# Optimization experiments

Measured on AMD Instinct MI355X. Metric: run time of the kernel, lower is better.

The kernel has to match this reference:

```python
import jax, jax.numpy as jnp
import numpy as np

H, D = 16, 64  # num_attention_heads, attention_head_size
BASE = 10000.0

def _rope(q, k, seq_len):
    # RotaryPositionalEmbedding: inv_freq over arange(0, D, 2); emb = cat(freqs, freqs)
    inv_freq = 1.0 / (BASE ** (jnp.arange(0, D, 2, dtype=jnp.float32) / D))  # [D/2]=32
    pos = jnp.arange(seq_len, dtype=jnp.float32)
    freqs = jnp.outer(pos, inv_freq)            # [S, 32]; equals cos_emb[..., :d]
    cos, sin = jnp.cos(freqs), jnp.sin(freqs)   # [S, 32]
    d = D // 2                                   # 32: only first half of head dim rotated
    half = d // 2                                # 16: internal rotate-half within rot part
    def rot(x):  # x: [B, H, S, D]
        xr, xp = x[..., :d], x[..., d:]
        swapped = jnp.concatenate([xr[..., half:], xr[..., :half]], axis=-1)
        xr2 = xr * cos - swapped * sin
        return jnp.concatenate([xr2, xp], axis=-1)
    return rot(q), rot(k)

def setup_inputs() -> dict:
    key = jax.random.key(0)
    ks = jax.random.split(key, 9)
    B, S, E = 2, 2048, 1024
    std = 0.02  # initializer_range
    inp = {"hidden_states": jax.random.normal(ks[0], (B, S, E), jnp.float32)}
    for i, n in enumerate(["q", "k", "v", "d"]):
        inp[f"W{n}"] = jax.random.normal(ks[1 + 2 * i], (E, E), jnp.float32) * std
        inp[f"b{n}"] = jnp.zeros((E,), jnp.float32)
    return inp

def reference(hidden_states, Wq, bq, Wk, bk, Wv, bv, Wd, bd):
    B, S, E = hidden_states.shape
    def heads(x):  # [B,S,E] -> [B,H,S,D]
        return x.reshape(B, S, H, D).transpose(0, 2, 1, 3)
    q = heads(hidden_states @ Wq + bq)
    k = heads(hidden_states @ Wk + bk)
    v = heads(hidden_states @ Wv + bv)
    q, k = _rope(q, k, S)
    scores = jnp.einsum("bhqd,bhkd->bhqk", q, k) / jnp.sqrt(jnp.float32(D))
    causal = jnp.tril(jnp.ones((S, S), dtype=bool))
    scores = jnp.where(causal, scores, -jnp.inf)
    probs = jax.nn.softmax(scores, axis=-1)
    ctx = jnp.einsum("bhqk,bhkd->bhqd", probs, v)
    ctx = ctx.transpose(0, 2, 1, 3).reshape(B, S, E)
    return ctx @ Wd + bd
```

## Files before the change

### kernel.cpp

```cpp
#include <hip/hip_runtime.h>
#include <stdint.h>

typedef __bf16 bf8 __attribute__((ext_vector_type(8)));
typedef float f4 __attribute__((ext_vector_type(4)));
typedef float f16v __attribute__((ext_vector_type(16)));
typedef unsigned short us8 __attribute__((ext_vector_type(8)));
typedef unsigned short us4 __attribute__((ext_vector_type(4)));

#define MFMA16(a, b, c) __builtin_amdgcn_mfma_f32_16x16x32_bf16(a, b, c, 0, 0, 0)
#define MFMA32(a, b, c) __builtin_amdgcn_mfma_f32_32x32x16_bf16(a, b, c, 0, 0, 0)

__device__ __forceinline__ unsigned short f2b(float f) {
  union { float f; unsigned u; } x; x.f = f;
  unsigned u = x.u;
  u += 0x7fffu + ((u >> 16) & 1u);
  return (unsigned short)(u >> 16);
}

__device__ __forceinline__ unsigned pk2(float a, float b) {
  union { float f; unsigned u; } ua, ub; ua.f = a; ub.f = b;
  return __builtin_amdgcn_perm(ub.u + 0x8000u, ua.u + 0x8000u, 0x07060302u);
}

__device__ __forceinline__ void gload16(const void* g, void* l) {
  __builtin_amdgcn_global_load_lds(
      (const __attribute__((address_space(1))) void*)g,
      (__attribute__((address_space(3))) void*)l, 16, 0, 0);
}

__global__ __launch_bounds__(256) void prep_kernel(
    const float* __restrict__ W0, const float* __restrict__ W1,
    const float* __restrict__ W2, const float* __restrict__ W3,
    unsigned short* __restrict__ T0, unsigned short* __restrict__ T1,
    unsigned short* __restrict__ T2, unsigned short* __restrict__ T3,
    const float* __restrict__ hid, unsigned short* __restrict__ hb) {
  if (blockIdx.z == 4) {
    int bi = blockIdx.x + 32 * blockIdx.y;
#pragma unroll
    for (int k = 0; k < 4; ++k) {
      int i = bi * 1024 + k * 256 + threadIdx.x;
      float4 v = ((const float4*)hid)[i];
      us4 r = { f2b(v.x), f2b(v.y), f2b(v.z), f2b(v.w) };
      *(us4*)(hb + (size_t)i * 4) = r;
    }
    return;
  }
  const float* W; unsigned short* Wt;
  if (blockIdx.z == 0)      { W = W0; Wt = T0; }
  else if (blockIdx.z == 1) { W = W1; Wt = T1; }
  else if (blockIdx.z == 2) { W = W2; Wt = T2; }
  else                      { W = W3; Wt = T3; }
  __shared__ float tile[32][33];
  int tx = threadIdx.x & 31, ty = threadIdx.x >> 5;
  int kb = blockIdx.x * 32, nb = blockIdx.y * 32;
#pragma unroll
  for (int j = 0; j < 32; j += 8)
    tile[ty + j][tx] = W[(size_t)(kb + ty + j) * 1024 + nb + tx];
  __syncthreads();
#pragma unroll
  for (int j = 0; j < 32; j += 8)
    Wt[(size_t)(nb + ty + j) * 1024 + kb + tx] = f2b(tile[tx][ty + j]);
}

__global__ __launch_bounds__(256) void gemm_qkv_kernel(
    const unsigned short* __restrict__ X,
    const unsigned short* __restrict__ Wqt, const unsigned short* __restrict__ Wkt,
    const unsigned short* __restrict__ Wvt,
    const float* __restrict__ bq, const float* __restrict__ bk,
    const float* __restrict__ bv,
    unsigned short* __restrict__ Qo, unsigned short* __restrict__ Ko,
    unsigned short* __restrict__ Vo) {
  const unsigned short* Wt; const float* bias; unsigned short* out;
  if (blockIdx.z == 0)      { Wt = Wqt; bias = bq; out = Qo; }
  else if (blockIdx.z == 1) { Wt = Wkt; bias = bk; out = Ko; }
  else                      { Wt = Wvt; bias = bv; out = Vo; }

  __shared__ unsigned short As[128 * 32];
  __shared__ unsigned short Bs[128 * 32];
  const int t = threadIdx.x;
  const int wave = t >> 6, lane = t & 63, quad = lane >> 4, l16 = lane & 15;
  const int wm = (wave >> 1) * 64, wn = (wave & 1) * 64;
  const int m0 = blockIdx.y * 128, n0 = blockIdx.x * 128;

  f4 acc[4][4];
#pragma unroll
  for (int mi = 0; mi < 4; ++mi)
#pragma unroll
    for (int ni = 0; ni < 4; ++ni) acc[mi][ni] = (f4)0.0f;

  for (int k0 = 0; k0 < 1024; k0 += 32) {
    __syncthreads();
#pragma unroll
    for (int it = 0; it < 2; ++it) {
      int chunk = it * 256 + wave * 64 + lane;
      int row = chunk >> 2, c = chunk & 3;
      gload16(&X[(size_t)(m0 + row) * 1024 + k0 + c * 8],
              &As[(size_t)(it * 256 + wave * 64) * 8]);
      gload16(&Wt[(size_t)(n0 + row) * 1024 + k0 + c * 8],
              &Bs[(size_t)(it * 256 + wave * 64) * 8]);
    }
    __syncthreads();
    bf8 a[4], b[4];
#pragma unroll
    for (int mi = 0; mi < 4; ++mi)
      a[mi] = *(const bf8*)&As[(wm + mi * 16 + l16) * 32 + quad * 8];
#pragma unroll
    for (int ni = 0; ni < 4; ++ni)
      b[ni] = *(const bf8*)&Bs[(wn + ni * 16 + l16) * 32 + quad * 8];
#pragma unroll
    for (int mi = 0; mi < 4; ++mi)
#pragma unroll
      for (int ni = 0; ni < 4; ++ni)
        acc[mi][ni] = MFMA16(a[mi], b[ni], acc[mi][ni]);
  }

  float biasv[4];
#pragma unroll
  for (int ni = 0; ni < 4; ++ni) biasv[ni] = bias[n0 + wn + ni * 16 + l16];

  if (blockIdx.z < 2) {
    const float kr = 13.287712379549449f / 32.0f;
    const float f0 = exp2f(-(float)l16 * kr);
    const float f1 = exp2f(-(float)(l16 + 16) * kr);
    const float qs = (blockIdx.z == 0) ? 0.18033688011112042f : 1.0f;
#pragma unroll
    for (int mi = 0; mi < 4; ++mi) {
#pragma unroll
      for (int r = 0; r < 4; ++r) {
        int m = m0 + wm + mi * 16 + quad * 4 + r;
        float s = (float)(m & 2047);
        float s0, c0, s1, c1;
        __sincosf(s * f0, &s0, &c0);
        __sincosf(s * f1, &s1, &c1);
        float v0 = acc[mi][0][r] + biasv[0];
        float v1 = acc[mi][1][r] + biasv[1];
        acc[mi][0][r] = (v0 * c0 - v1 * s0) * qs;
        acc[mi][1][r] = (v1 * c1 - v0 * s1) * qs;
        acc[mi][2][r] = (acc[mi][2][r] + biasv[2]) * qs;
        acc[mi][3][r] = (acc[mi][3][r] + biasv[3]) * qs;
      }
    }
#pragma unroll
    for (int ni = 0; ni < 4; ++ni) {
      int n = n0 + wn + ni * 16 + l16;
      int h = n >> 6, d = n & 63;
#pragma unroll
      for (int mi = 0; mi < 4; ++mi) {
#pragma unroll
        for (int r = 0; r < 4; ++r) {
          int m = m0 + wm + mi * 16 + quad * 4 + r;
          int b_ = m >> 11, s = m & 2047;
          out[(size_t)(((b_ << 4) | h) * 2048 + s) * 64 + d] = f2b(acc[mi][ni][r]);
        }
      }
    }
  } else {
#pragma unroll
    for (int ni = 0; ni < 4; ++ni) {
      int n = n0 + wn + ni * 16 + l16;
      int h = n >> 6, d = n & 63;
#pragma unroll
      for (int mi = 0; mi < 4; ++mi) {
        int m = m0 + wm + mi * 16 + quad * 4;
        int b_ = m >> 11, s = m & 2047;
        us4 w = { f2b(acc[mi][ni][0] + biasv[ni]), f2b(acc[mi][ni][1] + biasv[ni]),
                  f2b(acc[mi][ni][2] + biasv[ni]), f2b(acc[mi][ni][3] + biasv[ni]) };
        *(us4*)&out[((size_t)(((b_ << 4) | h) * 64 + d)) * 2048 + s] = w;
      }
    }
  }
}

__global__ __launch_bounds__(256, 2) void flash_attn_kernel(
    const unsigned short* __restrict__ Q, const unsigned short* __restrict__ K,
    const unsigned short* __restrict__ Vt, unsigned short* __restrict__ ctx) {
  const int t = threadIdx.x;
  const int lane = t & 63;
  const int wave = t >> 6, l32 = lane & 31, hl = lane >> 5;

  const int id = blockIdx.x;
  const int bh = id & 31;
  const int j = id >> 5;
  const int qt = (j >> 3) ? (15 - (j & 7)) : (j & 7);
  const int qbase = qt * 128;
  const int b = bh >> 4, h = bh & 15;

  const unsigned short* Qh = Q + (size_t)bh * 2048 * 64;
  const unsigned short* Kh = K + (size_t)bh * 2048 * 64;
  const unsigned short* Vh = Vt + (size_t)bh * 64 * 2048;

  const int wrow0 = qbase + wave * 32;
  const int q = wrow0 + l32;

  bf8 qb[4];
#pragma unroll
  for (int c = 0; c < 4; ++c)
    qb[c] = *(const bf8*)&Qh[(size_t)q * 64 + c * 16 + hl * 8];

  f16v o0 = (f16v)0.0f, o1 = (f16v)0.0f;
  float sum = 0.0f;

  bf8 kfA[2][4], kfB[2][4], vf[2][4];
  const int nkw = (wrow0 >> 6) + 1;

  auto loadK = [&](bf8 (&kf)[2][4], int k0) {
#pragma unroll
    for (int mt = 0; mt < 2; ++mt)
#pragma unroll
      for (int c = 0; c < 4; ++c)
        kf[mt][c] = *(const bf8*)&Kh[(size_t)(k0 + mt * 32 + l32) * 64 + c * 16 + hl * 8];
  };

  auto step = [&](int kt, bf8 (&kf)[2][4]) {
    const int k0 = kt * 64;
#pragma unroll
    for (int dt = 0; dt < 2; ++dt)
#pragma unroll
      for (int c = 0; c < 4; ++c)
        vf[dt][c] = *(const bf8*)&Vh[(size_t)(dt * 32 + l32) * 2048 + k0 + c * 16 + hl * 8];

    f16v s0 = (f16v)0.0f, s1 = (f16v)0.0f;
#pragma unroll
    for (int c = 0; c < 4; ++c) {
      s0 = MFMA32(kf[0][c], qb[c], s0);
      s1 = MFMA32(kf[1][c], qb[c], s1);
    }
    if (kt == nkw - 1) {
#pragma unroll
      for (int gg = 0; gg < 4; ++gg)
#pragma unroll
        for (int i = 0; i < 4; ++i) {
          int kk = k0 + gg * 8 + hl * 4 + i;
          if (kk > q) s0[gg * 4 + i] = -3e38f;
          if (kk + 32 > q) s1[gg * 4 + i] = -3e38f;
        }
    }
    uint2 pd2[8];
#pragma unroll
    for (int gg = 0; gg < 4; ++gg) {
      float p0 = exp2f(s0[gg * 4 + 0]), p1 = exp2f(s0[gg * 4 + 1]);
      float p2 = exp2f(s0[gg * 4 + 2]), p3 = exp2f(s0[gg * 4 + 3]);
      sum += (p0 + p1) + (p2 + p3);
      pd2[gg].x = pk2(p0, p1); pd2[gg].y = pk2(p2, p3);
      float r0 = exp2f(s1[gg * 4 + 0]), r1 = exp2f(s1[gg * 4 + 1]);
      float r2 = exp2f(s1[gg * 4 + 2]), r3 = exp2f(s1[gg * 4 + 3]);
      sum += (r0 + r1) + (r2 + r3);
      pd2[4 + gg].x = pk2(r0, r1); pd2[4 + gg].y = pk2(r2, r3);
    }
    uint4 fr[4];
#pragma unroll
    for (int c = 0; c < 4; ++c) {
      uint2 lo = pd2[2 * c], hi = pd2[2 * c + 1];
      unsigned sx = hl ? lo.x : hi.x, sy = hl ? lo.y : hi.y;
      unsigned rx = __shfl_xor(sx, 32), ry = __shfl_xor(sy, 32);
      fr[c].x = hl ? rx : lo.x;
      fr[c].y = hl ? ry : lo.y;
      fr[c].z = hl ? hi.x : rx;
      fr[c].w = hl ? hi.y : ry;
    }
#pragma unroll
    for (int c = 0; c < 4; ++c) {
      union { uint4 u; bf8 v; } pv; pv.u = fr[c];
      o0 = MFMA32(vf[0][c], pv.v, o0);
      o1 = MFMA32(vf[1][c], pv.v, o1);
    }
  };

  loadK(kfA, 0);
  int kt = 0;
  while (true) {
    if (kt + 1 < nkw) loadK(kfB, (kt + 1) * 64);
    step(kt, kfA);
    ++kt; if (kt >= nkw) break;
    if (kt + 1 < nkw) loadK(kfA, (kt + 1) * 64);
    step(kt, kfB);
    ++kt; if (kt >= nkw) break;
  }

  float lrow = sum + __shfl_xor(sum, 32);
  float inv = 1.0f / lrow;
#pragma unroll
  for (int gg = 0; gg < 4; ++gg) {
    int d0 = gg * 8 + hl * 4;
    us4 w0 = { f2b(o0[gg * 4 + 0] * inv), f2b(o0[gg * 4 + 1] * inv),
               f2b(o0[gg * 4 + 2] * inv), f2b(o0[gg * 4 + 3] * inv) };
    *(us4*)&ctx[((size_t)(b * 2048 + q)) * 1024 + h * 64 + d0] = w0;
    us4 w1 = { f2b(o1[gg * 4 + 0] * inv), f2b(o1[gg * 4 + 1] * inv),
               f2b(o1[gg * 4 + 2] * inv), f2b(o1[gg * 4 + 3] * inv) };
    *(us4*)&ctx[((size_t)(b * 2048 + q)) * 1024 + h * 64 + 32 + d0] = w1;
  }
}

__global__ __launch_bounds__(256) void gemm_out_kernel(
    const unsigned short* __restrict__ A,
    const unsigned short* __restrict__ Wt,
    const float* __restrict__ bias, float* __restrict__ out) {
  __shared__ unsigned short As[64 * 32];
  __shared__ unsigned short Bs[128 * 32];
  const int t = threadIdx.x;
  const int wave = t >> 6, lane = t & 63, quad = lane >> 4, l16 = lane & 15;
  const int wm = (wave & 1) * 32, wn = (wave >> 1) * 64;
  const int m0 = blockIdx.y * 64, n0 = blockIdx.x * 128;

  f4 acc[2][4];
#pragma unroll
  for (int mi = 0; mi < 2; ++mi)
#pragma unroll
    for (int ni = 0; ni < 4; ++ni) acc[mi][ni] = (f4)0.0f;

  for (int k0 = 0; k0 < 1024; k0 += 32) {
    __syncthreads();
    {
      int chunk = wave * 64 + lane;
      int row = chunk >> 2, c = chunk & 3;
      gload16(&A[(size_t)(m0 + row) * 1024 + k0 + c * 8],
              &As[(size_t)(wave * 64) * 8]);
#pragma unroll
      for (int it = 0; it < 2; ++it) {
        int ch = it * 256 + wave * 64 + lane;
        int rw = ch >> 2, cc = ch & 3;
        gload16(&Wt[(size_t)(n0 + rw) * 1024 + k0 + cc * 8],
                &Bs[(size_t)(it * 256 + wave * 64) * 8]);
      }
    }
    __syncthreads();
    bf8 a[2], b[4];
#pragma unroll
    for (int mi = 0; mi < 2; ++mi)
      a[mi] = *(const bf8*)&As[(wm + mi * 16 + l16) * 32 + quad * 8];
#pragma unroll
    for (int ni = 0; ni < 4; ++ni)
      b[ni] = *(const bf8*)&Bs[(wn + ni * 16 + l16) * 32 + quad * 8];
#pragma unroll
    for (int mi = 0; mi < 2; ++mi)
#pragma unroll
      for (int ni = 0; ni < 4; ++ni)
        acc[mi][ni] = MFMA16(a[mi], b[ni], acc[mi][ni]);
  }
#pragma unroll
  for (int ni = 0; ni < 4; ++ni) {
    int n = n0 + wn + ni * 16 + l16;
    float bv_ = bias[n];
#pragma unroll
    for (int mi = 0; mi < 2; ++mi) {
#pragma unroll
      for (int r = 0; r < 4; ++r) {
        int m = m0 + wm + mi * 16 + quad * 4 + r;
        out[(size_t)m * 1024 + n] = acc[mi][ni][r] + bv_;
      }
    }
  }
}

extern "C" void kernel_launch(void* const* d_in, const int* in_sizes, int n_in,
                              void* d_out, int out_size, void* d_ws, size_t ws_size,
                              hipStream_t stream) {
  const float* hidden = (const float*)d_in[0];
  const float* Wq = (const float*)d_in[1];
  const float* bq = (const float*)d_in[2];
  const float* Wk = (const float*)d_in[3];
  const float* bk = (const float*)d_in[4];
  const float* Wv = (const float*)d_in[5];
  const float* bv = (const float*)d_in[6];
  const float* Wd = (const float*)d_in[7];
  const float* bd = (const float*)d_in[8];
  float* out = (float*)d_out;

  char* ws = (char*)d_ws;
  unsigned short* Xb  = (unsigned short*)(ws);
  unsigned short* Wqt = (unsigned short*)(ws + ( 8ull << 20));
  unsigned short* Wkt = (unsigned short*)(ws + (10ull << 20));
  unsigned short* Wvt = (unsigned short*)(ws + (12ull << 20));
  unsigned short* Wdt = (unsigned short*)(ws + (14ull << 20));
  unsigned short* Qb  = (unsigned short*)(ws + (16ull << 20));
  unsigned short* Kb  = (unsigned short*)(ws + (24ull << 20));
  unsigned short* Vb  = (unsigned short*)(ws + (32ull << 20));
  unsigned short* Cb  = (unsigned short*)(ws + (40ull << 20));

  prep_kernel<<<dim3(32, 32, 5), 256, 0, stream>>>(
      Wq, Wk, Wv, Wd, Wqt, Wkt, Wvt, Wdt, hidden, Xb);
  gemm_qkv_kernel<<<dim3(8, 32, 3), 256, 0, stream>>>(
      Xb, Wqt, Wkt, Wvt, bq, bk, bv, Qb, Kb, Vb);
  flash_attn_kernel<<<512, 256, 0, stream>>>(Qb, Kb, Vb, Cb);
  gemm_out_kernel<<<dim3(8, 64), 256, 0, stream>>>(Cb, Wdt, bd, out);
}
```

Before: 223.4 us.

## Split attention KV range across wave pairs and use permlane32 swap

```diff
diff --git a/kernel.cpp b/kernel.cpp
--- a/kernel.cpp
+++ b/kernel.cpp
@@ -20,6 +20,10 @@
 __device__ __forceinline__ unsigned pk2(float a, float b) {
   union { float f; unsigned u; } ua, ub; ua.f = a; ub.f = b;
   return __builtin_amdgcn_perm(ub.u + 0x8000u, ua.u + 0x8000u, 0x07060302u);
+}
+
+__device__ __forceinline__ void plswap(unsigned &a, unsigned &b) {
+  asm("v_permlane32_swap_b32 %0, %1" : "+v"(a), "+v"(b));
 }
 
 __device__ __forceinline__ void gload16(const void* g, void* l) {
@@ -171,25 +175,28 @@
   }
 }
 
-__global__ __launch_bounds__(256, 2) void flash_attn_kernel(
+__global__ __launch_bounds__(256, 4) void flash_attn_kernel(
     const unsigned short* __restrict__ Q, const unsigned short* __restrict__ K,
     const unsigned short* __restrict__ Vt, unsigned short* __restrict__ ctx) {
+  __shared__ __align__(16) float osh[2][64][36];
+  __shared__ float lsh[2][64];
   const int t = threadIdx.x;
   const int lane = t & 63;
   const int wave = t >> 6, l32 = lane & 31, hl = lane >> 5;
+  const int sub = wave >> 1;
+  const int kh  = wave & 1;
 
   const int id = blockIdx.x;
   const int bh = id & 31;
   const int j = id >> 5;
-  const int qt = (j >> 3) ? (15 - (j & 7)) : (j & 7);
-  const int qbase = qt * 128;
+  const int qt = (j & 16) ? (31 - (j & 15)) : (j & 15);
   const int b = bh >> 4, h = bh & 15;
 
   const unsigned short* Qh = Q + (size_t)bh * 2048 * 64;
   const unsigned short* Kh = K + (size_t)bh * 2048 * 64;
   const unsigned short* Vh = Vt + (size_t)bh * 64 * 2048;
 
-  const int wrow0 = qbase + wave * 32;
+  const int wrow0 = qt * 64 + sub * 32;
   const int q = wrow0 + l32;
 
   bf8 qb[4];
@@ -201,7 +208,9 @@
   float sum = 0.0f;
 
   bf8 kfA[2][4], kfB[2][4], vf[2][4];
-  const int nkw = (wrow0 >> 6) + 1;
+  const int nk = qt + 1;
+  const int kb = kh ? (nk >> 1) : 0;
+  const int ke = kh ? nk : (nk >> 1);
 
   auto loadK = [&](bf8 (&kf)[2][4], int k0) {
 #pragma unroll
@@ -225,7 +234,7 @@
       s0 = MFMA32(kf[0][c], qb[c], s0);
       s1 = MFMA32(kf[1][c], qb[c], s1);
     }
-    if (kt == nkw - 1) {
+    if (kt == nk - 1) {
 #pragma unroll
       for (int gg = 0; gg < 4; ++gg)
 #pragma unroll
@@ -250,13 +259,11 @@
     uint4 fr[4];
 #pragma unroll
     for (int c = 0; c < 4; ++c) {
-      uint2 lo = pd2[2 * c], hi = pd2[2 * c + 1];
-      unsigned sx = hl ? lo.x : hi.x, sy = hl ? lo.y : hi.y;
-      unsigned rx = __shfl_xor(sx, 32), ry = __shfl_xor(sy, 32);
-      fr[c].x = hl ? rx : lo.x;
-      fr[c].y = hl ? ry : lo.y;
-      fr[c].z = hl ? hi.x : rx;
-      fr[c].w = hl ? hi.y : ry;
+      unsigned ax = pd2[2 * c].x, bx = pd2[2 * c + 1].x;
+      unsigned ay = pd2[2 * c].y, by = pd2[2 * c + 1].y;
+      plswap(ax, bx);
+      plswap(ay, by);
+      fr[c].x = ax; fr[c].y = ay; fr[c].z = bx; fr[c].w = by;
     }
 #pragma unroll
     for (int c = 0; c < 4; ++c) {
@@ -266,28 +273,46 @@
     }
   };
 
-  loadK(kfA, 0);
-  int kt = 0;
-  while (true) {
-    if (kt + 1 < nkw) loadK(kfB, (kt + 1) * 64);
-    step(kt, kfA);
-    ++kt; if (kt >= nkw) break;
-    if (kt + 1 < nkw) loadK(kfA, (kt + 1) * 64);
-    step(kt, kfB);
-    ++kt; if (kt >= nkw) break;
-  }
-
-  float lrow = sum + __shfl_xor(sum, 32);
-  float inv = 1.0f / lrow;
-#pragma unroll
-  for (int gg = 0; gg < 4; ++gg) {
-    int d0 = gg * 8 + hl * 4;
-    us4 w0 = { f2b(o0[gg * 4 + 0] * inv), f2b(o0[gg * 4 + 1] * inv),
-               f2b(o0[gg * 4 + 2] * inv), f2b(o0[gg * 4 + 3] * inv) };
-    *(us4*)&ctx[((size_t)(b * 2048 + q)) * 1024 + h * 64 + d0] = w0;
-    us4 w1 = { f2b(o1[gg * 4 + 0] * inv), f2b(o1[gg * 4 + 1] * inv),
-               f2b(o1[gg * 4 + 2] * inv), f2b(o1[gg * 4 + 3] * inv) };
-    *(us4*)&ctx[((size_t)(b * 2048 + q)) * 1024 + h * 64 + 32 + d0] = w1;
+  if (kb < ke) {
+    loadK(kfA, kb * 64);
+    int kt = kb;
+    while (true) {
+      if (kt + 1 < ke) loadK(kfB, (kt + 1) * 64);
+      step(kt, kfA);
+      ++kt; if (kt >= ke) break;
+      if (kt + 1 < ke) loadK(kfA, (kt + 1) * 64);
+      step(kt, kfB);
+      ++kt; if (kt >= ke) break;
+    }
+  }
+
+  float lpart = sum + __shfl_xor(sum, 32);
+
+  if (kh == 0) {
+#pragma unroll
+    for (int gg = 0; gg < 4; ++gg) {
+      f4 w0 = { o0[gg * 4 + 0], o0[gg * 4 + 1], o0[gg * 4 + 2], o0[gg * 4 + 3] };
+      *(f4*)&osh[sub][lane][gg * 4] = w0;
+      f4 w1 = { o1[gg * 4 + 0], o1[gg * 4 + 1], o1[gg * 4 + 2], o1[gg * 4 + 3] };
+      *(f4*)&osh[sub][lane][16 + gg * 4] = w1;
+    }
+    lsh[sub][lane] = lpart;
+  }
+  __syncthreads();
+  if (kh == 1) {
+    float inv = 1.0f / (lpart + lsh[sub][lane]);
+#pragma unroll
+    for (int gg = 0; gg < 4; ++gg) {
+      int d0 = gg * 8 + hl * 4;
+      f4 a0 = *(f4*)&osh[sub][lane][gg * 4];
+      f4 a1 = *(f4*)&osh[sub][lane][16 + gg * 4];
+      us4 w0 = { f2b((o0[gg * 4 + 0] + a0[0]) * inv), f2b((o0[gg * 4 + 1] + a0[1]) * inv),
+                 f2b((o0[gg * 4 + 2] + a0[2]) * inv), f2b((o0[gg * 4 + 3] + a0[3]) * inv) };
+      *(us4*)&ctx[((size_t)(b * 2048 + q)) * 1024 + h * 64 + d0] = w0;
+      us4 w1 = { f2b((o1[gg * 4 + 0] + a1[0]) * inv), f2b((o1[gg * 4 + 1] + a1[1]) * inv),
+                 f2b((o1[gg * 4 + 2] + a1[2]) * inv), f2b((o1[gg * 4 + 3] + a1[3]) * inv) };
+      *(us4*)&ctx[((size_t)(b * 2048 + q)) * 1024 + h * 64 + 32 + d0] = w1;
+    }
   }
 }
 
@@ -381,6 +406,6 @@
       Wq, Wk, Wv, Wd, Wqt, Wkt, Wvt, Wdt, hidden, Xb);
   gemm_qkv_kernel<<<dim3(8, 32, 3), 256, 0, stream>>>(
       Xb, Wqt, Wkt, Wvt, bq, bk, bv, Qb, Kb, Vb);
-  flash_attn_kernel<<<512, 256, 0, stream>>>(Qb, Kb, Vb, Cb);
+  flash_attn_kernel<<<1024, 256, 0, stream>>>(Qb, Kb, Vb, Cb);
   gemm_out_kernel<<<dim3(8, 64), 256, 0, stream>>>(Cb, Wdt, bd, out);
 }
```

New measurement: 323.7 us. +44.9%, slower.
